# Kernel tuning notes

Hardware: AMD Instinct MI355X
Metric: run time of the kernel (lower is better)

The kernel has to match this reference:

```python
import jax, jax.numpy as jnp
import numpy as np
from jax import lax


def causal_dwconv(x, w, b):
    # x: (b, l, d); w: (k, 1, d) in WIO layout with feature_group_count=d; b: (d,)
    k = w.shape[0]
    y = lax.conv_general_dilated(
        x, w,
        window_strides=(1,),
        padding=[(k - 1, 0)],  # left pad only => causal, equals torch pad=k-1 then slice [:l]
        dimension_numbers=("NWC", "WIO", "NWC"),
        feature_group_count=x.shape[-1],
    )
    return y + b


def setup_inputs() -> dict:
    key = jax.random.key(0)
    ks = jax.random.split(key, 7)
    b, l, d = 4, 4096, 1024
    k1, k2 = 3, 128
    s1 = 1.0 / np.sqrt(k1)  # torch Conv1d init bound ~ 1/sqrt(in_ch/groups * k)
    s2 = 1.0 / np.sqrt(k2)
    sp = 1.0 / np.sqrt(d)
    return {
        "u": jax.random.normal(ks[0], (b, l, d), dtype=jnp.float32),
        "w1": jax.random.normal(ks[1], (k1, 1, d), dtype=jnp.float32) * s1,
        "b1": jax.random.normal(ks[2], (d,), dtype=jnp.float32) * s1,
        "w2": jax.random.normal(ks[3], (k2, 1, d), dtype=jnp.float32) * s2,
        "b2": jax.random.normal(ks[4], (d,), dtype=jnp.float32) * s2,
        "Wp": jax.random.normal(ks[5], (d, d), dtype=jnp.float32) * sp,
        "bp": jax.random.normal(ks[6], (d,), dtype=jnp.float32) * sp,
    }


def reference(u, w1, b1, w2, b2, Wp, bp):
    # conv1 -> silu -> conv2
    h = jax.nn.silu(causal_dwconv(u, w1, b1))
    u_conv2 = causal_dwconv(h, w2, b2)
    # linear projection (torch Linear: u @ Wp.T + bp) -> silu
    u_proj = jax.nn.silu(jnp.einsum("bld,ed->ble", u, Wp) + bp)
    y = u_conv2.astype(jnp.float32) * u_proj.astype(jnp.float32)
    return y.astype(u.dtype)
```

## Files before the change

### kernel.cpp

```cpp
#include <hip/hip_runtime.h>
#include <cstdint>
#include <cstddef>

#define D     1024
#define LSEQ  4096
#define BATCH 4
#define MROWS (BATCH * LSEQ)

typedef __attribute__((ext_vector_type(8))) __bf16 bf16x8;
typedef __attribute__((ext_vector_type(4))) float  f32x4;

__device__ __forceinline__ ushort f2bf(float f) {
  union { float f; uint32_t u; } v; v.f = f;
  uint32_t u = v.u;
  return (ushort)((u + 0x7fffu + ((u >> 16) & 1u)) >> 16);
}
__device__ __forceinline__ float bf2f(ushort h) {
  union { uint32_t u; float f; } v; v.u = ((uint32_t)h) << 16; return v.f;
}
__device__ __forceinline__ float silu_f(float x) { return x / (1.f + expf(-x)); }

__device__ __forceinline__ void gl_lds16(const void* g, void* l) {
  __builtin_amdgcn_global_load_lds(
      (const __attribute__((address_space(1))) void*)g,
      (__attribute__((address_space(3))) void*)l, 16, 0, 0);
}

__global__ __launch_bounds__(256) void cvt_wp(const float* __restrict__ s,
                                              ushort* __restrict__ d) {
  const int i = (blockIdx.x * 256 + threadIdx.x) * 4;
  const float4 v = *reinterpret_cast<const float4*>(&s[i]);
  ushort4 o;
  o.x = f2bf(v.x); o.y = f2bf(v.y); o.z = f2bf(v.z); o.w = f2bf(v.w);
  *reinterpret_cast<ushort4*>(&d[i]) = o;
}

#define TL1 64
__global__ __launch_bounds__(256) void conv1_silu_cvt(
    const float* __restrict__ u, const float* __restrict__ w1,
    const float* __restrict__ b1, ushort* __restrict__ h,
    ushort* __restrict__ ubf) {
  const int c4 = threadIdx.x * 4;
  const int b  = blockIdx.y;
  const int l0 = blockIdx.x * TL1;
  const size_t base = ((size_t)b * LSEQ) * D + c4;
  const float4 wa = *reinterpret_cast<const float4*>(&w1[c4]);
  const float4 wb = *reinterpret_cast<const float4*>(&w1[D + c4]);
  const float4 wc = *reinterpret_cast<const float4*>(&w1[2 * D + c4]);
  const float4 bi = *reinterpret_cast<const float4*>(&b1[c4]);
  float4 x0 = {0.f, 0.f, 0.f, 0.f}, x1 = {0.f, 0.f, 0.f, 0.f};
  if (l0 >= 2) x0 = *reinterpret_cast<const float4*>(&u[base + (size_t)(l0 - 2) * D]);
  if (l0 >= 1) x1 = *reinterpret_cast<const float4*>(&u[base + (size_t)(l0 - 1) * D]);
  #pragma unroll 4
  for (int l = l0; l < l0 + TL1; ++l) {
    const float4 x2 = *reinterpret_cast<const float4*>(&u[base + (size_t)l * D]);
    ushort4 ho, uo;
    ho.x = f2bf(silu_f(fmaf(x0.x, wa.x, fmaf(x1.x, wb.x, fmaf(x2.x, wc.x, bi.x)))));
    ho.y = f2bf(silu_f(fmaf(x0.y, wa.y, fmaf(x1.y, wb.y, fmaf(x2.y, wc.y, bi.y)))));
    ho.z = f2bf(silu_f(fmaf(x0.z, wa.z, fmaf(x1.z, wb.z, fmaf(x2.z, wc.z, bi.z)))));
    ho.w = f2bf(silu_f(fmaf(x0.w, wa.w, fmaf(x1.w, wb.w, fmaf(x2.w, wc.w, bi.w)))));
    uo.x = f2bf(x2.x); uo.y = f2bf(x2.y); uo.z = f2bf(x2.z); uo.w = f2bf(x2.w);
    *reinterpret_cast<ushort4*>(&h[base + (size_t)l * D])   = ho;
    *reinterpret_cast<ushort4*>(&ubf[base + (size_t)l * D]) = uo;
    x0 = x1; x1 = x2;
  }
}

#define BM 128
#define BN 128
#define BK 64
__global__ __launch_bounds__(256) void gemm_bias_silu(
    const ushort* __restrict__ A, const ushort* __restrict__ B,
    const float* __restrict__ bp, float* __restrict__ out) {
  __shared__ __align__(16) ushort lsA[BM][BK];
  __shared__ __align__(16) ushort lsB[BN][BK];
  const int tid  = threadIdx.x;
  const int wave = tid >> 6, lane = tid & 63;
  const int m0 = blockIdx.x * BM;
  const int n0 = blockIdx.y * BN;
  const int wr = (wave >> 1) * 64;
  const int wc = (wave & 1) * 64;
  const int fr = lane & 15;
  const int fk = (lane >> 4) * 8;
  char* ldsA = (char*)&lsA[0][0];
  char* ldsB = (char*)&lsB[0][0];

  f32x4 acc[4][4];
  #pragma unroll
  for (int i = 0; i < 4; ++i)
    #pragma unroll
    for (int j = 0; j < 4; ++j) acc[i][j] = f32x4{0.f, 0.f, 0.f, 0.f};

  for (int k0 = 0; k0 < D; k0 += BK) {
    #pragma unroll
    for (int q = 0; q < 4; ++q) {
      const int o = (wave * 4 + q) * 1024 + lane * 16;
      const int r = o >> 7, ce = (o & 127) >> 1;
      gl_lds16(&A[(size_t)(m0 + r) * D + k0 + ce], ldsA + o);
      gl_lds16(&B[(size_t)(n0 + r) * D + k0 + ce], ldsB + o);
    }
    __syncthreads();
    #pragma unroll
    for (int kk = 0; kk < 2; ++kk) {
      bf16x8 af[4], bfr[4];
      #pragma unroll
      for (int i = 0; i < 4; ++i)
        af[i] = *reinterpret_cast<const bf16x8*>(&lsA[wr + i * 16 + fr][kk * 32 + fk]);
      #pragma unroll
      for (int j = 0; j < 4; ++j)
        bfr[j] = *reinterpret_cast<const bf16x8*>(&lsB[wc + j * 16 + fr][kk * 32 + fk]);
      #pragma unroll
      for (int i = 0; i < 4; ++i)
        #pragma unroll
        for (int j = 0; j < 4; ++j)
          acc[i][j] = __builtin_amdgcn_mfma_f32_16x16x32_bf16(af[i], bfr[j],
                                                              acc[i][j], 0, 0, 0);
    }
    __syncthreads();
  }
  const int ccol  = lane & 15;
  const int rbase = (lane >> 4) * 4;
  #pragma unroll
  for (int i = 0; i < 4; ++i) {
    #pragma unroll
    for (int j = 0; j < 4; ++j) {
      const int gn  = n0 + wc + j * 16 + ccol;
      const float bv = bp[gn];
      #pragma unroll
      for (int r = 0; r < 4; ++r) {
        const int gm = m0 + wr + i * 16 + rbase + r;
        out[(size_t)gm * D + gn] = silu_f(acc[i][j][r] + bv);
      }
    }
  }
}

#define C2CH   64
#define C2TL   128
#define C2ROWS 255
__global__ __launch_bounds__(256, 3) void conv2_mul(
    const ushort* __restrict__ h, const float* __restrict__ w2,
    const float* __restrict__ b2, float* __restrict__ out) {
  __shared__ ushort hsb[C2ROWS * C2CH];
  __shared__ ushort wsb[C2CH * 130];
  const int tid = threadIdx.x;
  const int c0  = blockIdx.x * C2CH;
  const int L0  = blockIdx.y * C2TL;
  const int b   = blockIdx.z;
  const ushort* hb = h + ((size_t)b * LSEQ) * D;

  {
    const int sr = tid >> 4, sc = (tid & 15) * 4;
    #pragma unroll
    for (int pass = 0; pass < 16; ++pass) {
      const int r = pass * 16 + sr;
      if (r < C2ROWS) {
        const int g = L0 - 127 + r;
        unsigned long long v = 0ull;
        if (g >= 0)
          v = *reinterpret_cast<const unsigned long long*>(
                  &hb[(size_t)g * D + c0 + sc]);
        *reinterpret_cast<unsigned long long*>(&hsb[r * C2CH + sc]) = v;
      }
    }
  }
  {
    #pragma unroll
    for (int p = 0; p < 8; ++p) {
      const int idx = p * 256 + tid;
      const int t = idx >> 4, ch4 = (idx & 15) * 4;
      const float4 wv =
          *reinterpret_cast<const float4*>(&w2[(size_t)t * D + c0 + ch4]);
      wsb[(ch4 + 0) * 130 + t] = f2bf(wv.x);
      wsb[(ch4 + 1) * 130 + t] = f2bf(wv.y);
      wsb[(ch4 + 2) * 130 + t] = f2bf(wv.z);
      wsb[(ch4 + 3) * 130 + t] = f2bf(wv.w);
    }
  }
  __syncthreads();

  const int c   = tid & 63;
  const int ls0 = (tid >> 6) * 32;
  const float bias = b2[c0 + c];
  float* ob = out + ((size_t)b * LSEQ) * D + c0 + c;
  const ushort* hrow = &hsb[ls0 * C2CH + c];
  const char*   wrow = (const char*)&wsb[c * 130];

  float acc[32];
  #pragma unroll
  for (int r = 0; r < 32; ++r) acc[r] = 0.f;
  float hh[47];
  #pragma unroll
  for (int q = 0; q < 47; ++q) hh[q] = bf2f(hrow[q * C2CH]);

  #pragma unroll 1
  for (int it = 0; it < 2; ++it) {
    #pragma unroll
    for (int tb2 = 0; tb2 < 4; ++tb2) {
      #pragma unroll
      for (int i2 = 0; i2 < 8; ++i2) {
        const uint32_t wp = *reinterpret_cast<const uint32_t*>(
            wrow + (size_t)(it * 64 + tb2 * 16 + i2 * 2) * 2);
        union { uint32_t u; float f; } wl, wh;
        wl.u = wp << 16; wh.u = wp & 0xffff0000u;
        #pragma unroll
        for (int r = 0; r < 32; ++r) {
          acc[r] = fmaf(wl.f, hh[i2 * 2 + r], acc[r]);
          acc[r] = fmaf(wh.f, hh[i2 * 2 + 1 + r], acc[r]);
        }
      }
      #pragma unroll
      for (int q = 0; q < 31; ++q) hh[q] = hh[q + 16];
      const int nb = it * 64 + tb2 * 16 + 16;
      #pragma unroll
      for (int q = 31; q < 47; ++q)
        hh[q] = bf2f(hrow[(size_t)(nb + q) * C2CH]);
    }
  }

  #pragma unroll
  for (int r = 0; r < 32; ++r) {
    const size_t p = (size_t)(L0 + ls0 + r) * D;
    const float pj = ob[p];
    ob[p] = (acc[r] + bias) * pj;
  }
}

extern "C" void kernel_launch(void* const* d_in, const int* in_sizes, int n_in,
                              void* d_out, int out_size, void* d_ws,
                              size_t ws_size, hipStream_t stream) {
  const float* u  = (const float*)d_in[0];
  const float* w1 = (const float*)d_in[1];
  const float* b1 = (const float*)d_in[2];
  const float* w2 = (const float*)d_in[3];
  const float* b2 = (const float*)d_in[4];
  const float* Wp = (const float*)d_in[5];
  const float* bp = (const float*)d_in[6];
  float* out = (float*)d_out;

  char* ws = (char*)d_ws;
  ushort* h    = (ushort*)(ws);
  ushort* ubf  = (ushort*)(ws + (size_t)33554432);
  ushort* wpbf = (ushort*)(ws + (size_t)67108864);

  cvt_wp<<<dim3(D * D / 1024), 256, 0, stream>>>(Wp, wpbf);
  conv1_silu_cvt<<<dim3(LSEQ / TL1, BATCH), 256, 0, stream>>>(
      u, w1, b1, h, ubf);
  gemm_bias_silu<<<dim3(MROWS / BM, D / BN), 256, 0, stream>>>(
      ubf, wpbf, bp, out);
  conv2_mul<<<dim3(D / C2CH, LSEQ / C2TL, BATCH), 256, 0, stream>>>(
      h, w2, b2, out);
}
```

Measured before the change: 302.3 us.

## Retune conv1 tiling, swap GEMM grid order, restructure conv2 register blocking

conv1 now takes 8 rows per block instead of 64 and fully unrolls its loop, giving many more blocks. The GEMM grid is transposed so consecutive blocks walk along N and share the same A row-panel in cache. conv2 loads its h tile with 16-byte stores and splits each thread's 32-row accumulator into two passes of 16 rows, prefetching the projection values first. This lowers register pressure, which can raise occupancy, at the cost of reloading the h window and the weights twice.

```diff
diff --git a/kernel.cpp b/kernel.cpp
--- a/kernel.cpp
+++ b/kernel.cpp
@@ -35,7 +35,7 @@
   *reinterpret_cast<ushort4*>(&d[i]) = o;
 }
 
-#define TL1 64
+#define TL1 8
 __global__ __launch_bounds__(256) void conv1_silu_cvt(
     const float* __restrict__ u, const float* __restrict__ w1,
     const float* __restrict__ b1, ushort* __restrict__ h,
@@ -51,7 +51,7 @@
   float4 x0 = {0.f, 0.f, 0.f, 0.f}, x1 = {0.f, 0.f, 0.f, 0.f};
   if (l0 >= 2) x0 = *reinterpret_cast<const float4*>(&u[base + (size_t)(l0 - 2) * D]);
   if (l0 >= 1) x1 = *reinterpret_cast<const float4*>(&u[base + (size_t)(l0 - 1) * D]);
-  #pragma unroll 4
+  #pragma unroll
   for (int l = l0; l < l0 + TL1; ++l) {
     const float4 x2 = *reinterpret_cast<const float4*>(&u[base + (size_t)l * D]);
     ushort4 ho, uo;
@@ -76,8 +76,8 @@
   __shared__ __align__(16) ushort lsB[BN][BK];
   const int tid  = threadIdx.x;
   const int wave = tid >> 6, lane = tid & 63;
-  const int m0 = blockIdx.x * BM;
-  const int n0 = blockIdx.y * BN;
+  const int m0 = blockIdx.y * BM;
+  const int n0 = blockIdx.x * BN;
   const int wr = (wave >> 1) * 64;
   const int wc = (wave & 1) * 64;
   const int fr = lane & 15;
@@ -141,7 +141,7 @@
 __global__ __launch_bounds__(256, 3) void conv2_mul(
     const ushort* __restrict__ h, const float* __restrict__ w2,
     const float* __restrict__ b2, float* __restrict__ out) {
-  __shared__ ushort hsb[C2ROWS * C2CH];
+  __shared__ __align__(16) ushort hsb[C2ROWS * C2CH];
   __shared__ ushort wsb[C2CH * 130];
   const int tid = threadIdx.x;
   const int c0  = blockIdx.x * C2CH;
@@ -150,17 +150,18 @@
   const ushort* hb = h + ((size_t)b * LSEQ) * D;
 
   {
-    const int sr = tid >> 4, sc = (tid & 15) * 4;
-    #pragma unroll
-    for (int pass = 0; pass < 16; ++pass) {
-      const int r = pass * 16 + sr;
-      if (r < C2ROWS) {
+    char* hdst = (char*)hsb;
+    #pragma unroll
+    for (int pass = 0; pass < 8; ++pass) {
+      const int idx = pass * 4096 + tid * 16;
+      if (idx < C2ROWS * 128) {
+        const int r = idx >> 7;
         const int g = L0 - 127 + r;
-        unsigned long long v = 0ull;
+        int4 v = {0, 0, 0, 0};
         if (g >= 0)
-          v = *reinterpret_cast<const unsigned long long*>(
-                  &hb[(size_t)g * D + c0 + sc]);
-        *reinterpret_cast<unsigned long long*>(&hsb[r * C2CH + sc]) = v;
+          v = *reinterpret_cast<const int4*>(
+                  &hb[(size_t)g * D + c0 + ((idx & 127) >> 1)]);
+        *reinterpret_cast<int4*>(hdst + idx) = v;
       }
     }
   }
@@ -179,50 +180,54 @@
   }
   __syncthreads();
 
-  const int c   = tid & 63;
-  const int ls0 = (tid >> 6) * 32;
+  const int c = tid & 63;
+  const int q = tid >> 6;
   const float bias = b2[c0 + c];
   float* ob = out + ((size_t)b * LSEQ) * D + c0 + c;
-  const ushort* hrow = &hsb[ls0 * C2CH + c];
+  const ushort* hcol = &hsb[c];
   const char*   wrow = (const char*)&wsb[c * 130];
 
-  float acc[32];
-  #pragma unroll
-  for (int r = 0; r < 32; ++r) acc[r] = 0.f;
-  float hh[47];
-  #pragma unroll
-  for (int q = 0; q < 47; ++q) hh[q] = bf2f(hrow[q * C2CH]);
-
   #pragma unroll 1
-  for (int it = 0; it < 2; ++it) {
-    #pragma unroll
-    for (int tb2 = 0; tb2 < 4; ++tb2) {
+  for (int g2 = 0; g2 < 2; ++g2) {
+    const int ls0 = q * 16 + g2 * 64;
+    float pj[16];
+    #pragma unroll
+    for (int r = 0; r < 16; ++r)
+      pj[r] = ob[(size_t)(L0 + ls0 + r) * D];
+
+    float acc[16];
+    #pragma unroll
+    for (int r = 0; r < 16; ++r) acc[r] = 0.f;
+    float hh[31];
+    #pragma unroll
+    for (int qq = 0; qq < 31; ++qq)
+      hh[qq] = bf2f(hcol[(size_t)(ls0 + qq) * C2CH]);
+
+    #pragma unroll
+    for (int tb = 0; tb < 8; ++tb) {
       #pragma unroll
       for (int i2 = 0; i2 < 8; ++i2) {
         const uint32_t wp = *reinterpret_cast<const uint32_t*>(
-            wrow + (size_t)(it * 64 + tb2 * 16 + i2 * 2) * 2);
+            wrow + (size_t)(tb * 16 + i2 * 2) * 2);
         union { uint32_t u; float f; } wl, wh;
         wl.u = wp << 16; wh.u = wp & 0xffff0000u;
         #pragma unroll
-        for (int r = 0; r < 32; ++r) {
+        for (int r = 0; r < 16; ++r) {
           acc[r] = fmaf(wl.f, hh[i2 * 2 + r], acc[r]);
           acc[r] = fmaf(wh.f, hh[i2 * 2 + 1 + r], acc[r]);
         }
       }
-      #pragma unroll
-      for (int q = 0; q < 31; ++q) hh[q] = hh[q + 16];
-      const int nb = it * 64 + tb2 * 16 + 16;
-      #pragma unroll
-      for (int q = 31; q < 47; ++q)
-        hh[q] = bf2f(hrow[(size_t)(nb + q) * C2CH]);
-    }
-  }
-
-  #pragma unroll
-  for (int r = 0; r < 32; ++r) {
-    const size_t p = (size_t)(L0 + ls0 + r) * D;
-    const float pj = ob[p];
-    ob[p] = (acc[r] + bias) * pj;
+      if (tb < 7) {
+        #pragma unroll
+        for (int qq = 0; qq < 15; ++qq) hh[qq] = hh[qq + 16];
+        #pragma unroll
+        for (int qq = 15; qq < 31; ++qq)
+          hh[qq] = bf2f(hcol[(size_t)(ls0 + 16 * (tb + 1) + qq) * C2CH]);
+      }
+    }
+    #pragma unroll
+    for (int r = 0; r < 16; ++r)
+      ob[(size_t)(L0 + ls0 + r) * D] = (acc[r] + bias) * pj[r];
   }
 }
 
@@ -246,7 +251,7 @@
   cvt_wp<<<dim3(D * D / 1024), 256, 0, stream>>>(Wp, wpbf);
   conv1_silu_cvt<<<dim3(LSEQ / TL1, BATCH), 256, 0, stream>>>(
       u, w1, b1, h, ubf);
-  gemm_bias_silu<<<dim3(MROWS / BM, D / BN), 256, 0, stream>>>(
+  gemm_bias_silu<<<dim3(D / BN, MROWS / BM), 256, 0, stream>>>(
       ubf, wpbf, bp, out);
   conv2_mul<<<dim3(D / C2CH, LSEQ / C2TL, BATCH), 256, 0, stream>>>(
       h, w2, b2, out);
```

Measured after the change: 350.4 us. 1.16x slower.
